# Kernel tuning notes

Hardware: AMD Instinct MI355X
Metric: run time of the kernel (lower is better)

The kernel has to match this reference:

```python
import jax, jax.numpy as jnp
import numpy as np

NUM_HEADS = 8
LN_EPS = 1e-5


def _ln(x, g, b):
    mu = x.mean(-1, keepdims=True)
    xc = x - mu
    v = (xc * xc).mean(-1, keepdims=True)
    return xc * jax.lax.rsqrt(v + LN_EPS) * g + b


def setup_inputs() -> dict:
    key = jax.random.key(0)
    B, T, D, NI, NT = 16, 512, 256, 85, 77
    L, FF, TH = 2, 1024, 32
    ks = iter(jax.random.split(key, 40))
    def nrm(shape, std):
        return jax.random.normal(next(ks), shape, jnp.float32) * std
    inp = {
        'img_tokens': nrm((B, NI, D), 1.0),
        'text_tokens': nrm((B, NT, D), 1.0),
        'task_tokens': nrm((T, D), 0.02),
        'type_task': nrm((D,), 0.02),
        'type_img': nrm((D,), 0.02),
        'type_txt': nrm((D,), 0.02),
        'in_ln_g': jnp.ones((D,), jnp.float32), 'in_ln_b': jnp.zeros((D,), jnp.float32),
        'Wqkv': nrm((L, 3 * D, D), 1.0 / np.sqrt(D)), 'bqkv': jnp.zeros((L, 3 * D), jnp.float32),
        'Wo': nrm((L, D, D), 1.0 / np.sqrt(D)), 'bo': jnp.zeros((L, D), jnp.float32),
        'ln1_g': jnp.ones((L, D), jnp.float32), 'ln1_b': jnp.zeros((L, D), jnp.float32),
        'ln2_g': jnp.ones((L, D), jnp.float32), 'ln2_b': jnp.zeros((L, D), jnp.float32),
        'W1': nrm((L, FF, D), 1.0 / np.sqrt(D)), 'b1': jnp.zeros((L, FF), jnp.float32),
        'W2': nrm((L, D, FF), 1.0 / np.sqrt(FF)), 'b2': jnp.zeros((L, D), jnp.float32),
        'out_ln_g': jnp.ones((D,), jnp.float32), 'out_ln_b': jnp.zeros((D,), jnp.float32),
        'tw1': nrm((T, TH, D), 1.0 / np.sqrt(D)), 'tb1': jnp.zeros((T, TH), jnp.float32),
        'tw2': nrm((T, TH), 1.0 / np.sqrt(TH)), 'tb2': jnp.zeros((T,), jnp.float32),
        'text_mask': jnp.arange(NT)[None, :] < jax.random.randint(next(ks), (B, 1), 10, NT + 1),
        'labels': jax.random.randint(next(ks), (B, T), -1, 2),
    }
    return inp


def reference(img_tokens, text_tokens, task_tokens, type_task, type_img, type_txt,
              in_ln_g, in_ln_b, Wqkv, bqkv, Wo, bo, ln1_g, ln1_b, ln2_g, ln2_b,
              W1, b1, W2, b2, out_ln_g, out_ln_b, tw1, tb1, tw2, tb2,
              text_mask, labels):
    B, NI, D = img_tokens.shape
    T = task_tokens.shape[0]
    L = Wqkv.shape[0]
    hd = D // NUM_HEADS
    available = labels != -1                                   # (B, T)
    n_avail = available.sum(axis=1)                            # (B,)
    # Route B: stable-sort available task ids to the front (permutation per row)
    order = jnp.argsort((~available).astype(jnp.int32), axis=1, stable=True)  # (B, T)
    task_toks = task_tokens[order] + type_task                 # (B, T, D)
    seq = jnp.concatenate([task_toks, img_tokens + type_img, text_tokens + type_txt], axis=1)
    seq = _ln(seq, in_ln_g, in_ln_b)
    task_pad = jnp.arange(T)[None, :] >= n_avail[:, None]
    pad = jnp.concatenate([task_pad, jnp.zeros((B, NI), bool), ~text_mask], axis=1)
    bias = jnp.where(pad, -1e9, 0.0).astype(seq.dtype)[:, None, None, :]  # key-padding mask
    scale = 1.0 / np.sqrt(hd)
    S = seq.shape[1]
    for l in range(L):  # pre-LN transformer encoder layers (eval mode)
        h = _ln(seq, ln1_g[l], ln1_b[l])
        qkv = h @ Wqkv[l].T + bqkv[l]
        q, k, v = jnp.split(qkv, 3, axis=-1)
        q = q.reshape(B, S, NUM_HEADS, hd)
        k = k.reshape(B, S, NUM_HEADS, hd)
        v = v.reshape(B, S, NUM_HEADS, hd)
        scores = jnp.einsum('bqhd,bkhd->bhqk', q, k) * scale + bias
        attn = jax.nn.softmax(scores, axis=-1)
        o = jnp.einsum('bhqk,bkhd->bqhd', attn, v).reshape(B, S, D)
        seq = seq + o @ Wo[l].T + bo[l]
        h2 = _ln(seq, ln2_g[l], ln2_b[l])
        seq = seq + jax.nn.gelu(h2 @ W1[l].T + b1[l], approximate=False) @ W2[l].T + b2[l]
    task_out = _ln(seq[:, :T], out_ln_g, out_ln_b)             # (B, T, D)
    # undo the per-row permutation so task t's token sits at column t, then
    # apply all per-task towers as one grouped matmul (MoE dispatch/combine)
    y = jnp.zeros_like(task_out).at[jnp.arange(B)[:, None], order].set(task_out)
    hsz = jax.nn.relu(jnp.einsum('btd,thd->bth', y, tw1) + tb1[None])
    out = jnp.einsum('bth,th->bt', hsz, tw2) + tb2[None]
    return jnp.where(available, out, jnp.zeros((), out.dtype))
```

## Files before the change

kernel.cpp:

```cpp
#include <hip/hip_runtime.h>
#include <hip/hip_bf16.h>
#include <math.h>

constexpr int B_  = 16;
constexpr int T_  = 512;
constexpr int D_  = 256;
constexpr int NI_ = 85;
constexpr int NT_ = 77;
constexpr int S_  = T_ + NI_ + NT_;
constexpr int M_  = B_ * S_;
constexpr int FF_ = 1024;
constexpr int TH_ = 32;
constexpr int NH_ = 8;
constexpr int KT_ = 704;

constexpr float MASK_NEG = -30000.0f;

constexpr int N_FT = 26;
constexpr int OFF_[N_FT + 1] = {
    0,
    348160,
    663552,
    794624,
    794880,
    795136,
    795392,
    795648,
    795904,
    1189120,
    1190656,
    1321728,
    1322240,
    1322752,
    1323264,
    1323776,
    1324288,
    1848576,
    1850624,
    2374912,
    2375424,
    2375680,
    2375936,
    6570240,
    6586624,
    6603008,
    6603520
};
constexpr int TOTAL_ELEMS = OFF_[N_FT];

typedef __attribute__((ext_vector_type(8))) short bfrag;
typedef __attribute__((ext_vector_type(4))) float f32x4;

__device__ inline float bf2f(__hip_bfloat16 x) { return __bfloat162float(x); }
__device__ inline __hip_bfloat16 f2bf(float x) { return __float2bfloat16(x); }
__device__ inline float bfbits2f(unsigned short u) {
    unsigned int x = ((unsigned int)u) << 16;
    float f;
    __builtin_memcpy(&f, &x, 4);
    return f;
}
__device__ inline float wsum64(float v) {
    #pragma unroll
    for (int m = 32; m >= 1; m >>= 1) v += __shfl_xor(v, m, 64);
    return v;
}
__device__ inline bool is_f32_mode(const void* ln_g_raw) {
    return (*(const unsigned int*)ln_g_raw) == 0x3F800000u;
}

__device__ inline void gload_lds16(const __hip_bfloat16* g, __hip_bfloat16* l) {
#if defined(__has_builtin) && __has_builtin(__builtin_amdgcn_global_load_lds)
    __builtin_amdgcn_global_load_lds(
        (const __attribute__((address_space(1))) unsigned int*)g,
        (__attribute__((address_space(3))) unsigned int*)l, 16, 0, 0);
#else
    *reinterpret_cast<uint4*>(l) = *reinterpret_cast<const uint4*>(g);
#endif
}

struct Ptrs { const void* p[N_FT]; };

__global__ __launch_bounds__(256) void k_convert(Ptrs ptrs, __hip_bfloat16* __restrict__ canon) {
    int idx = blockIdx.x * 256 + threadIdx.x;
    if (idx >= TOTAL_ELEMS) return;
    bool f32 = is_f32_mode(ptrs.p[6]);
    int t = 0;
    #pragma unroll
    for (int i = 1; i < N_FT; i++) if (idx >= OFF_[i]) t = i;
    int local = idx - OFF_[t];
    if (f32) canon[idx] = f2bf(((const float*)ptrs.p[t])[local]);
    else     canon[idx] = ((const __hip_bfloat16*)ptrs.p[t])[local];
}

__global__ void k_prep(const int* __restrict__ labels, int* __restrict__ inv,
                       int* __restrict__ n_avail) {
    __shared__ int sc[T_];
    int b = blockIdx.x, t = threadIdx.x;
    int av = (labels[b * T_ + t] != -1) ? 1 : 0;
    sc[t] = av;
    __syncthreads();
    for (int off = 1; off < T_; off <<= 1) {
        int v = sc[t];
        int u = (t >= off) ? sc[t - off] : 0;
        __syncthreads();
        sc[t] = v + u;
        __syncthreads();
    }
    int incl  = sc[t];
    int excl  = incl - av;
    int total = sc[T_ - 1];
    inv[b * T_ + t] = av ? excl : (total + (t - excl));
    if (t == 0) n_avail[b] = total;
}

__global__ void k_build(const __hip_bfloat16* __restrict__ img,
                        const __hip_bfloat16* __restrict__ txt,
                        const __hip_bfloat16* __restrict__ task,
                        const __hip_bfloat16* __restrict__ ty_task,
                        const __hip_bfloat16* __restrict__ ty_img,
                        const __hip_bfloat16* __restrict__ ty_txt,
                        const __hip_bfloat16* __restrict__ g,
                        const __hip_bfloat16* __restrict__ bln,
                        const __hip_bfloat16* __restrict__ g1,
                        const __hip_bfloat16* __restrict__ b1,
                        const void* __restrict__ text_mask,
                        const int* __restrict__ inv,
                        const int* __restrict__ n_avail,
                        float* __restrict__ seq,
                        __hip_bfloat16* __restrict__ h1,
                        float* __restrict__ bias) {
    int blk = blockIdx.x;
    int b = blk / S_, j = blk % S_;
    int lane = threadIdx.x;

    int dest;
    float bias_v;
    const __hip_bfloat16* src;
    const __hip_bfloat16* tvec;
    if (j < T_) {
        dest = inv[b * T_ + j];
        src = task + (size_t)j * D_;
        tvec = ty_task;
        bias_v = (dest >= n_avail[b]) ? MASK_NEG : 0.f;
    } else if (j < T_ + NI_) {
        dest = j;
        src = img + (size_t)(b * NI_ + (j - T_)) * D_;
        tvec = ty_img;
        bias_v = 0.f;
    } else {
        int x2 = j - T_ - NI_;
        dest = j;
        src = txt + (size_t)(b * NT_ + x2) * D_;
        tvec = ty_txt;
        const unsigned char* mb = (const unsigned char*)text_mask;
        bool is_byte = (mb[1] != 0);
        int mv = is_byte ? (int)mb[b * NT_ + x2]
                         : ((const int*)text_mask)[b * NT_ + x2];
        bias_v = mv ? 0.f : MASK_NEG;
    }

    float x[4];
    float s = 0.f, ss = 0.f;
    #pragma unroll
    for (int i = 0; i < 4; i++) {
        int d = lane * 4 + i;
        x[i] = bf2f(src[d]) + bf2f(tvec[d]);
        s += x[i];
        ss += x[i] * x[i];
    }
    s = wsum64(s);
    ss = wsum64(ss);
    float mean = s * (1.f / D_);
    float var  = ss * (1.f / D_) - mean * mean;
    float r    = rsqrtf(fmaxf(var, 0.f) + 1e-5f);

    float y[4];
    float s2 = 0.f, ss2 = 0.f;
    float* orow = seq + ((size_t)b * S_ + dest) * D_;
    #pragma unroll
    for (int i = 0; i < 4; i++) {
        int d = lane * 4 + i;
        y[i] = (x[i] - mean) * r * bf2f(g[d]) + bf2f(bln[d]);
        orow[d] = y[i];
        s2 += y[i];
        ss2 += y[i] * y[i];
    }
    s2 = wsum64(s2);
    ss2 = wsum64(ss2);
    float mean2 = s2 * (1.f / D_);
    float var2  = ss2 * (1.f / D_) - mean2 * mean2;
    float r2    = rsqrtf(fmaxf(var2, 0.f) + 1e-5f);
    __hip_bfloat16 tmp[4];
    #pragma unroll
    for (int i = 0; i < 4; i++) {
        int d = lane * 4 + i;
        tmp[i] = f2bf((y[i] - mean2) * r2 * bf2f(g1[d]) + bf2f(b1[d]));
    }
    *reinterpret_cast<uint2*>(h1 + ((size_t)b * S_ + dest) * D_ + lane * 4) =
        *reinterpret_cast<uint2*>(tmp);
    if (lane == 0) bias[b * S_ + dest] = bias_v;
}

template <int GELU>
__global__ __launch_bounds__(256) void k_gemm(const __hip_bfloat16* __restrict__ A,
                                              const __hip_bfloat16* __restrict__ W,
                                              const __hip_bfloat16* __restrict__ bias,
                                              __hip_bfloat16* __restrict__ Cout,
                                              int Mm, int N, int K) {
    __shared__ __align__(16) unsigned char Sh[16384];
    __hip_bfloat16* As = (__hip_bfloat16*)Sh;
    __hip_bfloat16* Ws = (__hip_bfloat16*)(Sh + 8192);
    __hip_bfloat16* Es = (__hip_bfloat16*)Sh;

    int m0 = blockIdx.x * 64;
    int n0 = blockIdx.y * 64;
    int tid = threadIdx.x;
    int w = tid >> 6, lane = tid & 63;
    int lrow = lane & 15, quad = lane >> 4;

    f32x4 acc[4] = {};

    int row0 = tid >> 3, kq = (tid & 7) * 8;
    const __hip_bfloat16* Ar0 = A + (size_t)min(m0 + row0,      Mm - 1) * K + kq;
    const __hip_bfloat16* Ar1 = A + (size_t)min(m0 + row0 + 32, Mm - 1) * K + kq;
    const __hip_bfloat16* Wr0 = W + (size_t)(n0 + row0) * K + kq;
    const __hip_bfloat16* Wr1 = W + (size_t)(n0 + row0 + 32) * K + kq;
    __hip_bfloat16* Al0 = As + tid * 8;
    __hip_bfloat16* Al1 = As + (tid + 256) * 8;
    __hip_bfloat16* Wl0 = Ws + tid * 8;
    __hip_bfloat16* Wl1 = Ws + (tid + 256) * 8;

    for (int k0 = 0; k0 < K; k0 += 64) {
        __syncthreads();
        gload_lds16(Ar0 + k0, Al0);
        gload_lds16(Ar1 + k0, Al1);
        gload_lds16(Wr0 + k0, Wl0);
        gload_lds16(Wr1 + k0, Wl1);
        __syncthreads();

        #pragma unroll
        for (int ko = 0; ko < 2; ko++) {
            bfrag af = *reinterpret_cast<const bfrag*>(&As[(w * 16 + lrow) * 64 + ko * 32 + quad * 8]);
            #pragma unroll
            for (int nt = 0; nt < 4; nt++) {
                bfrag bf = *reinterpret_cast<const bfrag*>(&Ws[(nt * 16 + lrow) * 64 + ko * 32 + quad * 8]);
                acc[nt] = __builtin_amdgcn_mfma_f32_16x16x32_bf16(af, bf, acc[nt], 0, 0, 0);
            }
        }
    }
    __syncthreads();

    #pragma unroll
    for (int nt = 0; nt < 4; nt++) {
        int col = nt * 16 + lrow;
        float bv = bf2f(bias[n0 + col]);
        #pragma unroll
        for (int rg = 0; rg < 4; rg++) {
            int row = w * 16 + quad * 4 + rg;
            float v = acc[nt][rg] + bv;
            if (GELU) v = 0.5f * v * (1.f + erff(v * 0.70710678118654752f));
            Es[row * 72 + col] = f2bf(v);
        }
    }
    __syncthreads();

    #pragma unroll
    for (int i = 0; i < 2; i++) {
        int c = tid + i * 256;
        int row = c >> 3, off = (c & 7) * 8;
        int gm = m0 + row;
        if (gm < Mm) {
            uint4 v4 = *reinterpret_cast<const uint4*>(&Es[row * 72 + off]);
            *reinterpret_cast<uint4*>(&Cout[(size_t)gm * N + off + n0]) = v4;
        }
    }
}

template <int LNOUT>
__global__ __launch_bounds__(256) void k_gemm_lnres(const __hip_bfloat16* __restrict__ A,
                                                    const __hip_bfloat16* __restrict__ W,
                                                    const __hip_bfloat16* __restrict__ bias,
                                                    float* __restrict__ seq,
                                                    const __hip_bfloat16* __restrict__ lng,
                                                    const __hip_bfloat16* __restrict__ lnb,
                                                    __hip_bfloat16* __restrict__ lnout,
                                                    int K) {
    constexpr int N = 256;
    constexpr int ESTRIDE = 260;
    __shared__ __align__(16) unsigned char Sh[36864];
    __hip_bfloat16* As = (__hip_bfloat16*)Sh;
    __hip_bfloat16* Ws = (__hip_bfloat16*)(Sh + 4096);
    float*          Es = (float*)Sh;

    int m0 = blockIdx.x * 32;
    int tid = threadIdx.x;
    int w = tid >> 6, lane = tid & 63;
    int lrow = lane & 15, quad = lane >> 4;

    f32x4 acc[2][4] = {};

    int kq = (tid & 7) * 8;
    const __hip_bfloat16* Ar = A + (size_t)(m0 + (tid >> 3)) * K + kq;
    __hip_bfloat16* Al = As + tid * 8;
    const __hip_bfloat16* Wr[8];
    __hip_bfloat16* Wl[8];
    #pragma unroll
    for (int i = 0; i < 8; i++) {
        int c = tid + i * 256;
        Wr[i] = W + (size_t)(c >> 3) * K + kq;
        Wl[i] = Ws + c * 8;
    }

    for (int k0 = 0; k0 < K; k0 += 64) {
        __syncthreads();
        gload_lds16(Ar + k0, Al);
        #pragma unroll
        for (int i = 0; i < 8; i++) gload_lds16(Wr[i] + k0, Wl[i]);
        __syncthreads();

        #pragma unroll
        for (int ko = 0; ko < 2; ko++) {
            bfrag af[2], bf[4];
            #pragma unroll
            for (int mt = 0; mt < 2; mt++)
                af[mt] = *reinterpret_cast<const bfrag*>(&As[(mt * 16 + lrow) * 64 + ko * 32 + quad * 8]);
            #pragma unroll
            for (int nt = 0; nt < 4; nt++)
                bf[nt] = *reinterpret_cast<const bfrag*>(&Ws[(w * 64 + nt * 16 + lrow) * 64 + ko * 32 + quad * 8]);
            #pragma unroll
            for (int mt = 0; mt < 2; mt++)
                #pragma unroll
                for (int nt = 0; nt < 4; nt++)
                    acc[mt][nt] = __builtin_amdgcn_mfma_f32_16x16x32_bf16(af[mt], bf[nt], acc[mt][nt], 0, 0, 0);
        }
    }
    __syncthreads();

    #pragma unroll
    for (int nt = 0; nt < 4; nt++) {
        int col = w * 64 + nt * 16 + lrow;
        float bv = bf2f(bias[col]);
        #pragma unroll
        for (int mt = 0; mt < 2; mt++)
            #pragma unroll
            for (int rg = 0; rg < 4; rg++)
                Es[(mt * 16 + quad * 4 + rg) * ESTRIDE + col] = acc[mt][nt][rg] + bv;
    }
    __syncthreads();

    int row = tid >> 3, part = tid & 7;
    size_t gm = (size_t)(m0 + row);
    float* seqrow = seq + gm * N + part * 32;
    float t[32];
    float s = 0.f, ss = 0.f;
    #pragma unroll
    for (int j = 0; j < 8; j++) {
        float4 e = *reinterpret_cast<const float4*>(&Es[row * ESTRIDE + part * 32 + j * 4]);
        float4 r4 = *reinterpret_cast<const float4*>(&seqrow[j * 4]);
        float v0 = e.x + r4.x, v1 = e.y + r4.y, v2 = e.z + r4.z, v3 = e.w + r4.w;
        t[j * 4 + 0] = v0; t[j * 4 + 1] = v1; t[j * 4 + 2] = v2; t[j * 4 + 3] = v3;
        s += v0 + v1 + v2 + v3;
        ss += v0 * v0 + v1 * v1 + v2 * v2 + v3 * v3;
    }
    #pragma unroll
    for (int j = 0; j < 8; j++) {
        float4 o = make_float4(t[j * 4 + 0], t[j * 4 + 1], t[j * 4 + 2], t[j * 4 + 3]);
        *reinterpret_cast<float4*>(&seqrow[j * 4]) = o;
    }
    if (LNOUT) {
        #pragma unroll
        for (int mm = 4; mm >= 1; mm >>= 1) {
            s  += __shfl_xor(s,  mm, 8);
            ss += __shfl_xor(ss, mm, 8);
        }
        float mean = s * (1.f / N);
        float var  = ss * (1.f / N) - mean * mean;
        float r    = rsqrtf(fmaxf(var, 0.f) + 1e-5f);
        __hip_bfloat16 ob[32];
        #pragma unroll
        for (int j = 0; j < 32; j++) {
            int col = part * 32 + j;
            ob[j] = f2bf((t[j] - mean) * r * bf2f(lng[col]) + bf2f(lnb[col]));
        }
        #pragma unroll
        for (int j = 0; j < 4; j++)
            *reinterpret_cast<uint4*>(&lnout[gm * N + part * 32 + j * 8]) =
                *reinterpret_cast<const uint4*>(&ob[j * 8]);
    }
}

__global__ __launch_bounds__(256) void k_fattn(const __hip_bfloat16* __restrict__ qkv,
                                               const float* __restrict__ bias,
                                               __hip_bfloat16* __restrict__ out) {
    __shared__ __align__(16) __hip_bfloat16 Vt[2][32 * 72];
    __shared__ __align__(16) __hip_bfloat16 Ps[4][16 * 72];
    __shared__ float Bs[KT_];
    int b = blockIdx.z, h = blockIdx.y;
    int tid = threadIdx.x;
    int wave = tid >> 6, lane = tid & 63;
    int lrow = lane & 15, quad = lane >> 4;
    int q0 = blockIdx.x * 64 + wave * 16;

    const float scale = 0.17677669529663687f;
    const __hip_bfloat16* base = qkv + (size_t)b * S_ * 768;
    const float* brow = bias + b * S_;

    for (int i = tid; i < KT_; i += 256) Bs[i] = (i < S_) ? brow[i] : MASK_NEG;

    int qr = q0 + lrow; if (qr >= S_) qr = S_ - 1;
    bfrag qf = *reinterpret_cast<const bfrag*>(base + (size_t)qr * 768 + h * 32 + quad * 8);

    bfrag ones_f;
    #pragma unroll
    for (int i = 0; i < 8; i++) ((short*)&ones_f)[i] = (short)0x3F80;

    float m[4] = {-3e38f, -3e38f, -3e38f, -3e38f};
    f32x4 Lacc = {};
    f32x4 O[2] = {};

    int skey = lane;
    int sd   = wave * 8;

    const int ktiles = KT_ / 64;

    bfrag kf_cur[4], vv_cur;
    #pragma unroll
    for (int nt = 0; nt < 4; nt++) {
        int kr = min(nt * 16 + lrow, S_ - 1);
        kf_cur[nt] = *reinterpret_cast<const bfrag*>(base + (size_t)kr * 768 + 256 + h * 32 + quad * 8);
    }
    {
        int kr = min(skey, S_ - 1);
        vv_cur = *reinterpret_cast<const bfrag*>(base + (size_t)kr * 768 + 512 + h * 32 + sd);
    }

    for (int t = 0; t < ktiles; t++) {
        int k0 = t * 64;
        __hip_bfloat16* vb = Vt[t & 1];

        #pragma unroll
        for (int i = 0; i < 8; i++) vb[(sd + i) * 72 + skey] = ((const __hip_bfloat16*)&vv_cur)[i];
        __syncthreads();

        bfrag kf_nxt[4], vv_nxt;
        {
            int kb = k0 + 64;
            #pragma unroll
            for (int nt = 0; nt < 4; nt++) {
                int kr = min(kb + nt * 16 + lrow, S_ - 1);
                kf_nxt[nt] = *reinterpret_cast<const bfrag*>(base + (size_t)kr * 768 + 256 + h * 32 + quad * 8);
            }
            int kr = min(kb + skey, S_ - 1);
            vv_nxt = *reinterpret_cast<const bfrag*>(base + (size_t)kr * 768 + 512 + h * 32 + sd);
        }

        f32x4 sc4[4];
        #pragma unroll
        for (int nt = 0; nt < 4; nt++) {
            f32x4 z = {};
            sc4[nt] = __builtin_amdgcn_mfma_f32_16x16x32_bf16(qf, kf_cur[nt], z, 0, 0, 0);
            float bv = Bs[k0 + nt * 16 + lrow];
            #pragma unroll
            for (int rg = 0; rg < 4; rg++) sc4[nt][rg] = sc4[nt][rg] * scale + bv;
        }

        float alpha[4];
        #pragma unroll
        for (int rg = 0; rg < 4; rg++) {
            float rm = fmaxf(fmaxf(sc4[0][rg], sc4[1][rg]), fmaxf(sc4[2][rg], sc4[3][rg]));
            #pragma unroll
            for (int mm2 = 1; mm2 <= 8; mm2 <<= 1) rm = fmaxf(rm, __shfl_xor(rm, mm2, 64));
            float mn = fmaxf(m[rg], rm);
            alpha[rg] = __expf(m[rg] - mn);
            m[rg] = mn;
            #pragma unroll
            for (int nt = 0; nt < 4; nt++) sc4[nt][rg] = __expf(sc4[nt][rg] - mn);
        }
        #pragma unroll
        for (int rg = 0; rg < 4; rg++) {
            O[0][rg] *= alpha[rg];
            O[1][rg] *= alpha[rg];
            Lacc[rg] *= alpha[rg];
        }

        #pragma unroll
        for (int nt = 0; nt < 4; nt++)
            #pragma unroll
            for (int rg = 0; rg < 4; rg++)
                Ps[wave][(quad * 4 + rg) * 72 + nt * 16 + lrow] = f2bf(sc4[nt][rg]);

        bfrag ap0 = *reinterpret_cast<const bfrag*>(&Ps[wave][lrow * 72 + quad * 8]);
        bfrag ap1 = *reinterpret_cast<const bfrag*>(&Ps[wave][lrow * 72 + 32 + quad * 8]);
        #pragma unroll
        for (int dt = 0; dt < 2; dt++) {
            bfrag bv0 = *reinterpret_cast<const bfrag*>(&vb[(dt * 16 + lrow) * 72 + quad * 8]);
            bfrag bv1 = *reinterpret_cast<const bfrag*>(&vb[(dt * 16 + lrow) * 72 + 32 + quad * 8]);
            O[dt] = __builtin_amdgcn_mfma_f32_16x16x32_bf16(ap0, bv0, O[dt], 0, 0, 0);
            O[dt] = __builtin_amdgcn_mfma_f32_16x16x32_bf16(ap1, bv1, O[dt], 0, 0, 0);
        }
        Lacc = __builtin_amdgcn_mfma_f32_16x16x32_bf16(ap0, ones_f, Lacc, 0, 0, 0);
        Lacc = __builtin_amdgcn_mfma_f32_16x16x32_bf16(ap1, ones_f, Lacc, 0, 0, 0);

        #pragma unroll
        for (int nt = 0; nt < 4; nt++) kf_cur[nt] = kf_nxt[nt];
        vv_cur = vv_nxt;
    }

    #pragma unroll
    for (int rg = 0; rg < 4; rg++) {
        int qrow = q0 + quad * 4 + rg;
        if (qrow < S_) {
            float invl = 1.f / Lacc[rg];
            #pragma unroll
            for (int dt = 0; dt < 2; dt++)
                out[((size_t)b * S_ + qrow) * D_ + h * 32 + dt * 16 + lrow] = f2bf(O[dt][rg] * invl);
        }
    }
}

__global__ __launch_bounds__(256) void k_final(const float* __restrict__ seq,
                                               const int* __restrict__ inv,
                                               const int* __restrict__ labels,
                                               const __hip_bfloat16* __restrict__ g,
                                               const __hip_bfloat16* __restrict__ bb,
                                               const __hip_bfloat16* __restrict__ tw1,
                                               const __hip_bfloat16* __restrict__ tb1,
                                               const __hip_bfloat16* __restrict__ tw2,
                                               const __hip_bfloat16* __restrict__ tb2,
                                               const void* __restrict__ ln_g_raw,
                                               void* __restrict__ out) {
    int idx = blockIdx.x;
    int t = idx >> 4, b = idx & 15;
    int tid = threadIdx.x;
    bool f32o = is_f32_mode(ln_g_raw);

    int lab = labels[b * T_ + t];
    if (lab == -1) {
        if (tid == 0) {
            if (f32o) ((float*)out)[b * T_ + t] = 0.f;
            else      ((__hip_bfloat16*)out)[b * T_ + t] = f2bf(0.f);
        }
        return;
    }

    __shared__ float y[D_];
    __shared__ float hb[TH_];
    __shared__ float rs[4], rq[4];

    int row = inv[b * T_ + t];
    float x = seq[((size_t)b * S_ + row) * D_ + tid];
    float s1 = wsum64(x);
    float s2 = wsum64(x * x);
    int w = tid >> 6, lane = tid & 63;
    if (lane == 0) { rs[w] = s1; rq[w] = s2; }
    __syncthreads();
    float fs = rs[0] + rs[1] + rs[2] + rs[3];
    float fq = rq[0] + rq[1] + rq[2] + rq[3];
    float mean = fs * (1.f / D_);
    float var  = fq * (1.f / D_) - mean * mean;
    float r    = rsqrtf(fmaxf(var, 0.f) + 1e-5f);
    y[tid] = (x - mean) * r * bf2f(g[tid]) + bf2f(bb[tid]);
    __syncthreads();

    int hh = tid >> 3, part = tid & 7;
    const uint4* w4 = reinterpret_cast<const uint4*>(tw1 + ((size_t)t * TH_ + hh) * D_ + part * 32);
    float acc = 0.f;
    #pragma unroll
    for (int i = 0; i < 4; i++) {
        uint4 kv = w4[i];
        unsigned int wd[4] = {kv.x, kv.y, kv.z, kv.w};
        #pragma unroll
        for (int j2 = 0; j2 < 4; j2++) {
            acc += y[part * 32 + i * 8 + j2 * 2]     * bfbits2f((unsigned short)(wd[j2] & 0xffffu));
            acc += y[part * 32 + i * 8 + j2 * 2 + 1] * bfbits2f((unsigned short)(wd[j2] >> 16));
        }
    }
    #pragma unroll
    for (int mm = 4; mm >= 1; mm >>= 1) acc += __shfl_down(acc, mm, 8);
    if (part == 0) {
        float hz = acc + bf2f(tb1[t * TH_ + hh]);
        hz = fmaxf(hz, 0.f);
        hb[hh] = hz * bf2f(tw2[t * TH_ + hh]);
    }
    __syncthreads();
    if (tid == 0) {
        float o = bf2f(tb2[t]);
        #pragma unroll
        for (int i = 0; i < TH_; i++) o += hb[i];
        if (f32o) ((float*)out)[b * T_ + t] = o;
        else      ((__hip_bfloat16*)out)[b * T_ + t] = f2bf(o);
    }
}

extern "C" void kernel_launch(void* const* d_in, const int* in_sizes, int n_in,
                              void* d_out, int out_size, void* d_ws, size_t ws_size,
                              hipStream_t stream) {
    const void* tmask  = d_in[26];
    const int*  labels = (const int*)d_in[27];

    char* p = (char*)d_ws;
    auto alloc = [&](size_t bytes) {
        char* r = p;
        p += (bytes + 255) & ~size_t(255);
        return r;
    };
    __hip_bfloat16* canon  = (__hip_bfloat16*)alloc(sizeof(__hip_bfloat16) * (size_t)TOTAL_ELEMS);
    int*            inv     = (int*)alloc(sizeof(int) * B_ * T_);
    int*            n_avail = (int*)alloc(sizeof(int) * B_);
    float*          bias    = (float*)alloc(sizeof(float) * M_);
    float*          seqF    = (float*)alloc(sizeof(float) * (size_t)M_ * D_);
    __hip_bfloat16* bufA    = (__hip_bfloat16*)alloc(sizeof(__hip_bfloat16) * (size_t)M_ * D_);
    __hip_bfloat16* bufBig  = (__hip_bfloat16*)alloc(sizeof(__hip_bfloat16) * (size_t)M_ * FF_);

    Ptrs ptrs;
    for (int i = 0; i < N_FT; i++) ptrs.p[i] = d_in[i];
    hipLaunchKernelGGL(k_convert, dim3((TOTAL_ELEMS + 255) / 256), dim3(256), 0, stream,
                       ptrs, canon);

    const __hip_bfloat16* img      = canon + OFF_[0];
    const __hip_bfloat16* txt      = canon + OFF_[1];
    const __hip_bfloat16* task     = canon + OFF_[2];
    const __hip_bfloat16* ty_task  = canon + OFF_[3];
    const __hip_bfloat16* ty_img   = canon + OFF_[4];
    const __hip_bfloat16* ty_txt   = canon + OFF_[5];
    const __hip_bfloat16* in_ln_g  = canon + OFF_[6];
    const __hip_bfloat16* in_ln_b  = canon + OFF_[7];
    const __hip_bfloat16* Wqkv     = canon + OFF_[8];
    const __hip_bfloat16* bqkv     = canon + OFF_[9];
    const __hip_bfloat16* Wo       = canon + OFF_[10];
    const __hip_bfloat16* bo       = canon + OFF_[11];
    const __hip_bfloat16* ln1_g    = canon + OFF_[12];
    const __hip_bfloat16* ln1_b    = canon + OFF_[13];
    const __hip_bfloat16* ln2_g    = canon + OFF_[14];
    const __hip_bfloat16* ln2_b    = canon + OFF_[15];
    const __hip_bfloat16* W1       = canon + OFF_[16];
    const __hip_bfloat16* b1       = canon + OFF_[17];
    const __hip_bfloat16* W2       = canon + OFF_[18];
    const __hip_bfloat16* b2       = canon + OFF_[19];
    const __hip_bfloat16* out_ln_g = canon + OFF_[20];
    const __hip_bfloat16* out_ln_b = canon + OFF_[21];
    const __hip_bfloat16* tw1      = canon + OFF_[22];
    const __hip_bfloat16* tb1      = canon + OFF_[23];
    const __hip_bfloat16* tw2      = canon + OFF_[24];
    const __hip_bfloat16* tb2      = canon + OFF_[25];

    hipLaunchKernelGGL(k_prep, dim3(B_), dim3(T_), 0, stream, labels, inv, n_avail);
    hipLaunchKernelGGL(k_build, dim3(B_ * S_), dim3(64), 0, stream,
                       img, txt, task, ty_task, ty_img, ty_txt, in_ln_g, in_ln_b,
                       ln1_g, ln1_b, tmask, inv, n_avail, seqF, bufA, bias);

    const int mtiles = (M_ + 63) / 64;
    const int rtiles = M_ / 32;
    const int qtiles = (S_ + 63) / 64;

    for (int l = 0; l < 2; l++) {
        hipLaunchKernelGGL((k_gemm<0>), dim3(mtiles, 12), dim3(256), 0, stream,
                           bufA, Wqkv + (size_t)l * 3 * D_ * D_, bqkv + l * 3 * D_,
                           bufBig, M_, 3 * D_, D_);
        hipLaunchKernelGGL(k_fattn, dim3(qtiles, NH_, B_), dim3(256), 0, stream,
                           bufBig, bias, bufA);
        hipLaunchKernelGGL((k_gemm_lnres<1>), dim3(rtiles), dim3(256), 0, stream,
                           bufA, Wo + (size_t)l * D_ * D_, bo + l * D_, seqF,
                           ln2_g + l * D_, ln2_b + l * D_, bufA, D_);
        hipLaunchKernelGGL((k_gemm<1>), dim3(mtiles, 16), dim3(256), 0, stream,
                           bufA, W1 + (size_t)l * FF_ * D_, b1 + l * FF_,
                           bufBig, M_, FF_, D_);
        if (l == 0) {
            hipLaunchKernelGGL((k_gemm_lnres<1>), dim3(rtiles), dim3(256), 0, stream,
                               bufBig, W2 + (size_t)l * D_ * FF_, b2 + l * D_, seqF,
                               ln1_g + 1 * D_, ln1_b + 1 * D_, bufA, FF_);
        } else {
            hipLaunchKernelGGL((k_gemm_lnres<0>), dim3(rtiles), dim3(256), 0, stream,
                               bufBig, W2 + (size_t)l * D_ * FF_, b2 + l * D_, seqF,
                               (const __hip_bfloat16*)nullptr, (const __hip_bfloat16*)nullptr,
                               (__hip_bfloat16*)nullptr, FF_);
        }
    }

    hipLaunchKernelGGL(k_final, dim3(T_ * B_), dim3(256), 0, stream,
                       seqF, inv, labels, out_ln_g, out_ln_b,
                       tw1, tb1, tw2, tb2, d_in[6], d_out);
}
```

Baseline: 418.5 us.

## Widen GEMM N-tile to 128, skip fully masked key tiles in attention

The generic GEMM now computes a 64x128 output tile per block with 8 accumulators, which halves the grid and reuses each A fragment across twice as many MFMAs. The flash-attention kernel scans the bias row for 64-key tiles that are entirely masked and iterates only over live tiles, skipping their K/V loads and MFMAs. The final tower kernel's bf16 unpacking is also simplified to plain bit shifts. In exchange, the GEMM uses more LDS and registers, and attention pays a small setup cost for the tile-list scan.

```diff
diff --git a/kernel.cpp b/kernel.cpp
--- a/kernel.cpp
+++ b/kernel.cpp
@@ -13,6 +13,7 @@
 constexpr int TH_ = 32;
 constexpr int NH_ = 8;
 constexpr int KT_ = 704;
+constexpr int NKT_ = KT_ / 64;
 
 constexpr float MASK_NEG = -30000.0f;
 
@@ -53,12 +54,6 @@
 
 __device__ inline float bf2f(__hip_bfloat16 x) { return __bfloat162float(x); }
 __device__ inline __hip_bfloat16 f2bf(float x) { return __float2bfloat16(x); }
-__device__ inline float bfbits2f(unsigned short u) {
-    unsigned int x = ((unsigned int)u) << 16;
-    float f;
-    __builtin_memcpy(&f, &x, 4);
-    return f;
-}
 __device__ inline float wsum64(float v) {
     #pragma unroll
     for (int m = 32; m >= 1; m >>= 1) v += __shfl_xor(v, m, 64);
@@ -207,42 +202,47 @@
                                               const __hip_bfloat16* __restrict__ bias,
                                               __hip_bfloat16* __restrict__ Cout,
                                               int Mm, int N, int K) {
-    __shared__ __align__(16) unsigned char Sh[16384];
+    __shared__ __align__(16) unsigned char Sh[24576];
     __hip_bfloat16* As = (__hip_bfloat16*)Sh;
     __hip_bfloat16* Ws = (__hip_bfloat16*)(Sh + 8192);
     __hip_bfloat16* Es = (__hip_bfloat16*)Sh;
 
     int m0 = blockIdx.x * 64;
-    int n0 = blockIdx.y * 64;
+    int n0 = blockIdx.y * 128;
     int tid = threadIdx.x;
     int w = tid >> 6, lane = tid & 63;
     int lrow = lane & 15, quad = lane >> 4;
 
-    f32x4 acc[4] = {};
-
-    int row0 = tid >> 3, kq = (tid & 7) * 8;
-    const __hip_bfloat16* Ar0 = A + (size_t)min(m0 + row0,      Mm - 1) * K + kq;
-    const __hip_bfloat16* Ar1 = A + (size_t)min(m0 + row0 + 32, Mm - 1) * K + kq;
-    const __hip_bfloat16* Wr0 = W + (size_t)(n0 + row0) * K + kq;
-    const __hip_bfloat16* Wr1 = W + (size_t)(n0 + row0 + 32) * K + kq;
+    f32x4 acc[8] = {};
+
+    int kq = (tid & 7) * 8;
+    int arow = tid >> 3;
+    const __hip_bfloat16* Ar0 = A + (size_t)min(m0 + arow,      Mm - 1) * K + kq;
+    const __hip_bfloat16* Ar1 = A + (size_t)min(m0 + arow + 32, Mm - 1) * K + kq;
     __hip_bfloat16* Al0 = As + tid * 8;
     __hip_bfloat16* Al1 = As + (tid + 256) * 8;
-    __hip_bfloat16* Wl0 = Ws + tid * 8;
-    __hip_bfloat16* Wl1 = Ws + (tid + 256) * 8;
+    const __hip_bfloat16* Wr[4];
+    __hip_bfloat16* Wl[4];
+    #pragma unroll
+    for (int i = 0; i < 4; i++) {
+        int c = tid + i * 256;
+        Wr[i] = W + (size_t)(n0 + (c >> 3)) * K + kq;
+        Wl[i] = Ws + c * 8;
+    }
 
     for (int k0 = 0; k0 < K; k0 += 64) {
         __syncthreads();
         gload_lds16(Ar0 + k0, Al0);
         gload_lds16(Ar1 + k0, Al1);
-        gload_lds16(Wr0 + k0, Wl0);
-        gload_lds16(Wr1 + k0, Wl1);
+        #pragma unroll
+        for (int i = 0; i < 4; i++) gload_lds16(Wr[i] + k0, Wl[i]);
         __syncthreads();
 
         #pragma unroll
         for (int ko = 0; ko < 2; ko++) {
             bfrag af = *reinterpret_cast<const bfrag*>(&As[(w * 16 + lrow) * 64 + ko * 32 + quad * 8]);
             #pragma unroll
-            for (int nt = 0; nt < 4; nt++) {
+            for (int nt = 0; nt < 8; nt++) {
                 bfrag bf = *reinterpret_cast<const bfrag*>(&Ws[(nt * 16 + lrow) * 64 + ko * 32 + quad * 8]);
                 acc[nt] = __builtin_amdgcn_mfma_f32_16x16x32_bf16(af, bf, acc[nt], 0, 0, 0);
             }
@@ -251,7 +251,7 @@
     __syncthreads();
 
     #pragma unroll
-    for (int nt = 0; nt < 4; nt++) {
+    for (int nt = 0; nt < 8; nt++) {
         int col = nt * 16 + lrow;
         float bv = bf2f(bias[n0 + col]);
         #pragma unroll
@@ -259,19 +259,19 @@
             int row = w * 16 + quad * 4 + rg;
             float v = acc[nt][rg] + bv;
             if (GELU) v = 0.5f * v * (1.f + erff(v * 0.70710678118654752f));
-            Es[row * 72 + col] = f2bf(v);
-        }
-    }
-    __syncthreads();
-
-    #pragma unroll
-    for (int i = 0; i < 2; i++) {
+            Es[row * 136 + col] = f2bf(v);
+        }
+    }
+    __syncthreads();
+
+    #pragma unroll
+    for (int i = 0; i < 4; i++) {
         int c = tid + i * 256;
-        int row = c >> 3, off = (c & 7) * 8;
+        int row = c >> 4, off = (c & 15) * 8;
         int gm = m0 + row;
         if (gm < Mm) {
-            uint4 v4 = *reinterpret_cast<const uint4*>(&Es[row * 72 + off]);
-            *reinterpret_cast<uint4*>(&Cout[(size_t)gm * N + off + n0]) = v4;
+            uint4 v4 = *reinterpret_cast<const uint4*>(&Es[row * 136 + off]);
+            *reinterpret_cast<uint4*>(&Cout[(size_t)gm * N + n0 + off]) = v4;
         }
     }
 }
@@ -395,6 +395,9 @@
     __shared__ __align__(16) __hip_bfloat16 Vt[2][32 * 72];
     __shared__ __align__(16) __hip_bfloat16 Ps[4][16 * 72];
     __shared__ float Bs[KT_];
+    __shared__ int alive[NKT_];
+    __shared__ int tlist[NKT_ + 1];
+    __shared__ int nact_s;
     int b = blockIdx.z, h = blockIdx.y;
     int tid = threadIdx.x;
     int wave = tid >> 6, lane = tid & 63;
@@ -406,6 +409,20 @@
     const float* brow = bias + b * S_;
 
     for (int i = tid; i < KT_; i += 256) Bs[i] = (i < S_) ? brow[i] : MASK_NEG;
+    if (tid < NKT_) alive[tid] = 0;
+    __syncthreads();
+    for (int i = tid; i < KT_; i += 256)
+        if (Bs[i] != MASK_NEG) alive[i >> 6] = 1;
+    __syncthreads();
+    if (tid == 0) {
+        int n = 0;
+        for (int t = 0; t < NKT_; t++) if (alive[t]) tlist[n++] = t;
+        if (n == 0) { tlist[0] = 0; n = 1; }
+        tlist[n] = tlist[n - 1];
+        nact_s = n;
+    }
+    __syncthreads();
+    int nact = nact_s;
 
     int qr = q0 + lrow; if (qr >= S_) qr = S_ - 1;
     bfrag qf = *reinterpret_cast<const bfrag*>(base + (size_t)qr * 768 + h * 32 + quad * 8);
@@ -421,30 +438,29 @@
     int skey = lane;
     int sd   = wave * 8;
 
-    const int ktiles = KT_ / 64;
-
     bfrag kf_cur[4], vv_cur;
-    #pragma unroll
-    for (int nt = 0; nt < 4; nt++) {
-        int kr = min(nt * 16 + lrow, S_ - 1);
-        kf_cur[nt] = *reinterpret_cast<const bfrag*>(base + (size_t)kr * 768 + 256 + h * 32 + quad * 8);
-    }
     {
-        int kr = min(skey, S_ - 1);
+        int k0 = tlist[0] * 64;
+        #pragma unroll
+        for (int nt = 0; nt < 4; nt++) {
+            int kr = min(k0 + nt * 16 + lrow, S_ - 1);
+            kf_cur[nt] = *reinterpret_cast<const bfrag*>(base + (size_t)kr * 768 + 256 + h * 32 + quad * 8);
+        }
+        int kr = min(k0 + skey, S_ - 1);
         vv_cur = *reinterpret_cast<const bfrag*>(base + (size_t)kr * 768 + 512 + h * 32 + sd);
     }
 
-    for (int t = 0; t < ktiles; t++) {
-        int k0 = t * 64;
-        __hip_bfloat16* vb = Vt[t & 1];
-
-        #pragma unroll
-        for (int i = 0; i < 8; i++) vb[(sd + i) * 72 + skey] = ((const __hip_bfloat16*)&vv_cur)[i];
+    for (int i = 0; i < nact; i++) {
+        int k0 = tlist[i] * 64;
+        __hip_bfloat16* vb = Vt[i & 1];
+
+        #pragma unroll
+        for (int j = 0; j < 8; j++) vb[(sd + j) * 72 + skey] = ((const __hip_bfloat16*)&vv_cur)[j];
         __syncthreads();
 
         bfrag kf_nxt[4], vv_nxt;
         {
-            int kb = k0 + 64;
+            int kb = tlist[i + 1] * 64;
             #pragma unroll
             for (int nt = 0; nt < 4; nt++) {
                 int kr = min(kb + nt * 16 + lrow, S_ - 1);
@@ -571,8 +587,12 @@
         unsigned int wd[4] = {kv.x, kv.y, kv.z, kv.w};
         #pragma unroll
         for (int j2 = 0; j2 < 4; j2++) {
-            acc += y[part * 32 + i * 8 + j2 * 2]     * bfbits2f((unsigned short)(wd[j2] & 0xffffu));
-            acc += y[part * 32 + i * 8 + j2 * 2 + 1] * bfbits2f((unsigned short)(wd[j2] >> 16));
+            unsigned int lo = wd[j2] << 16, hi = wd[j2] & 0xffff0000u;
+            float flo, fhi;
+            __builtin_memcpy(&flo, &lo, 4);
+            __builtin_memcpy(&fhi, &hi, 4);
+            acc += y[part * 32 + i * 8 + j2 * 2] * flo;
+            acc += y[part * 32 + i * 8 + j2 * 2 + 1] * fhi;
         }
     }
     #pragma unroll
@@ -654,7 +674,7 @@
     const int qtiles = (S_ + 63) / 64;
 
     for (int l = 0; l < 2; l++) {
-        hipLaunchKernelGGL((k_gemm<0>), dim3(mtiles, 12), dim3(256), 0, stream,
+        hipLaunchKernelGGL((k_gemm<0>), dim3(mtiles, 6), dim3(256), 0, stream,
                            bufA, Wqkv + (size_t)l * 3 * D_ * D_, bqkv + l * 3 * D_,
                            bufBig, M_, 3 * D_, D_);
         hipLaunchKernelGGL(k_fattn, dim3(qtiles, NH_, B_), dim3(256), 0, stream,
@@ -662,7 +682,7 @@
         hipLaunchKernelGGL((k_gemm_lnres<1>), dim3(rtiles), dim3(256), 0, stream,
                            bufA, Wo + (size_t)l * D_ * D_, bo + l * D_, seqF,
                            ln2_g + l * D_, ln2_b + l * D_, bufA, D_);
-        hipLaunchKernelGGL((k_gemm<1>), dim3(mtiles, 16), dim3(256), 0, stream,
+        hipLaunchKernelGGL((k_gemm<1>), dim3(mtiles, 8), dim3(256), 0, stream,
                            bufA, W1 + (size_t)l * FF_ * D_, b1 + l * FF_,
                            bufBig, M_, FF_, D_);
         if (l == 0) {
```

New measurement: 403.4 us (median of 2 runs). 3.6% less time.
